# Kernel optimization log

Hardware: AMD Instinct MI355X
Metric: run time of the kernel (lower is better)

## Reference

```python
import jax, jax.numpy as jnp
import numpy as np

K = 8  # repeat(1,1,1,9) in the source forces k+1 == 9
LRELU_SLOPE = 0.01  # nn.LeakyReLU default negative slope


def knn_idx(x, k):
    """x: [B, C, N] -> indices of k nearest points [B, N, k] (largest neg sq dist)."""
    xx = jnp.sum(x * x, axis=1)                       # [B, N]
    inner = jnp.einsum('bcn,bcm->bnm', x, x)          # [B, N, N]
    neg_sq_dist = 2.0 * inner - xx[:, :, None] - xx[:, None, :]
    return jax.lax.top_k(neg_sq_dist, k)[1]           # [B, N, k]


def gather_neighbors(feat, idx):
    """feat: [B, C, N], idx: [B, N, k] -> [B, C, N, k] (grouping_operation)."""
    return jax.vmap(lambda f, i: f[:, i])(feat, idx)


def setup_inputs() -> dict:
    key = jax.random.key(0)
    k1, k2, k3 = jax.random.split(key, 3)
    B, C, N = 8, 128, 4096
    points = jax.random.normal(k1, (B, C, N), dtype=jnp.float32)
    # xavier_uniform-ish init for W [C, 1]
    limit = 1.414 * np.sqrt(6.0 / (C + 1))
    W = jax.random.uniform(k2, (C, 1), dtype=jnp.float32, minval=-limit, maxval=limit)
    conv2_w = jax.random.normal(k3, (C, C), dtype=jnp.float32) * 0.05
    return {"points": points, "W": W, "conv2_w": conv2_w}


def reference(points, W, conv2_w):
    # points: [B, C, N]
    shortcut = points
    # knn on raw (detached) features -> integer indices, no grad path
    idx = knn_idx(jax.lax.stop_gradient(points), K)            # [B, N, K]
    features = jax.nn.leaky_relu(points, LRELU_SLOPE)          # [B, C, N]
    grouped_points = gather_neighbors(features, idx)           # [B, C, N, K]
    center_points = features[:, :, :, None]                    # [B, C, N, 1]
    feats = jnp.concatenate([grouped_points, center_points], axis=3)  # [B, C, N, K+1]
    feats = jnp.transpose(feats, (0, 2, 3, 1))                 # [B, N, K+1, C]
    att = jnp.einsum('bnkc,co->bnko', feats, W)                # [B, N, K+1, 1]
    att = jax.nn.softmax(att, axis=2)                          # softmax over K+1 neighbors
    # repeat(1,1,1,9) then matmul: out[b,n,i,c] = att[b,n,i] * sum_j feats[b,n,j,c]
    # followed by mean over i -> mean_i(att) * sum_j(feats)
    s = jnp.sum(feats, axis=2)                                 # [B, N, C]
    out = jnp.mean(att, axis=2) * s                            # [B, N, C]
    out = jnp.transpose(out, (0, 2, 1)) + shortcut             # [B, C, N]
    # 1x1 conv residual branch on grouped neighbor features
    grouped_points_nn = jnp.einsum('oc,bcnk->bonk', conv2_w, grouped_points)  # [B, C, N, K]
    return (out, grouped_points_nn)
```

## Files before the change

kernel.cpp:

```cpp
#include <hip/hip_runtime.h>
#include <cstdint>
#include <cstddef>

#define BB_ 8
#define CC_ 128
#define NN_ 4096
#define KK_ 8

#define XX_OFF  0
#define IDX_OFF 32768
#define G_OFF   294912

__device__ __forceinline__ float lrelu(float v) { return v >= 0.f ? v : 0.01f * v; }

template <int S>
__device__ __forceinline__ void insert_tieup(float (&v)[S], int (&ix)[S], float d, int m) {
  if (d < v[S - 1]) return;
  bool bs[S];
#pragma unroll
  for (int s = 0; s < S; ++s) bs[s] = (v[s] > d);
#pragma unroll
  for (int s = S - 1; s >= 1; --s) {
    v[s]  = bs[s] ? v[s]  : (bs[s - 1] ? d : v[s - 1]);
    ix[s] = bs[s] ? ix[s] : (bs[s - 1] ? m : ix[s - 1]);
  }
  if (!bs[0]) { v[0] = d; ix[0] = m; }
}

template <int S>
__device__ __forceinline__ void insert_ti_desc(float (&v)[S], int (&ix)[S], float d, int m) {
  bool stay = (v[S - 1] > d) || (v[S - 1] == d && ix[S - 1] > m);
  if (stay) return;
  bool bs[S];
#pragma unroll
  for (int s = 0; s < S; ++s) bs[s] = (v[s] > d) || (v[s] == d && ix[s] > m);
#pragma unroll
  for (int s = S - 1; s >= 1; --s) {
    v[s]  = bs[s] ? v[s]  : (bs[s - 1] ? d : v[s - 1]);
    ix[s] = bs[s] ? ix[s] : (bs[s - 1] ? m : ix[s - 1]);
  }
  if (!bs[0]) { v[0] = d; ix[0] = m; }
}

__global__ void k_xx(const float* __restrict__ x, float* __restrict__ out1f) {
  int t = blockIdx.x * 256 + threadIdx.x;
  int b = t >> 12, n = t & (NN_ - 1);
  const float* p = x + ((size_t)b * CC_) * NN_ + n;
  float acc = 0.f;
  {
#pragma clang fp contract(off)
#pragma unroll
    for (int c = 0; c < CC_; ++c) {
      float v = p[(size_t)c * NN_];
      float v2 = v * v;
      acc = acc + v2;
    }
  }
  out1f[XX_OFF + t] = acc;
}

__global__ __launch_bounds__(256, 2) void k_knn(const float* __restrict__ x,
                                                float* __restrict__ out1f) {
  __shared__ __align__(16) float As[32][132];
  __shared__ __align__(16) union MB {
    float B[64][132];
    struct { float v[32 * 128]; int i[32 * 128]; } mg;
  } sb;
  __shared__ float xxm[64];

  const float* xxz = out1f + XX_OFF;
  int* idxz = (int*)(out1f + IDX_OFF);

  const int blk = blockIdx.x;
  const int b = blk >> 7;
  const int n0 = (blk & 127) << 5;
  const float* xb = x + ((size_t)b * CC_) * NN_;
  const int t = threadIdx.x;
  const int tr = t & 15, tc = t >> 4;

  {
    int r = t & 31, c0 = t >> 5;
    for (int c = c0; c < CC_; c += 8) As[r][c] = xb[(size_t)c * NN_ + n0 + r];
  }

  float xr[2];
#pragma unroll
  for (int i = 0; i < 2; ++i) xr[i] = xxz[(b << 12) + n0 + tr + 16 * i];

  float lv[2][8]; int li[2][8];
#pragma unroll
  for (int i = 0; i < 2; ++i)
#pragma unroll
    for (int s = 0; s < 8; ++s) { lv[i][s] = -INFINITY; li[i][s] = 0x7FFFFFFF; }

  for (int m0 = 0; m0 < NN_; m0 += 64) {
    __syncthreads();
    {
      int ml = t & 63, c1 = t >> 6;
      for (int c = c1; c < CC_; c += 4) sb.B[ml][c] = xb[(size_t)c * NN_ + m0 + ml];
      if (t < 64) xxm[t] = xxz[(b << 12) + m0 + t];
    }
    __syncthreads();

    float acc[2][4] = {};
#pragma unroll 8
    for (int cq = 0; cq < CC_; cq += 4) {
      float4 av[2], bv4[4];
#pragma unroll
      for (int i = 0; i < 2; ++i) av[i] = *reinterpret_cast<const float4*>(&As[tr + 16 * i][cq]);
#pragma unroll
      for (int j = 0; j < 4; ++j) bv4[j] = *reinterpret_cast<const float4*>(&sb.B[tc + 16 * j][cq]);
#pragma unroll
      for (int i = 0; i < 2; ++i)
#pragma unroll
        for (int j = 0; j < 4; ++j) {
          acc[i][j] = fmaf(av[i].x, bv4[j].x, acc[i][j]);
          acc[i][j] = fmaf(av[i].y, bv4[j].y, acc[i][j]);
          acc[i][j] = fmaf(av[i].z, bv4[j].z, acc[i][j]);
          acc[i][j] = fmaf(av[i].w, bv4[j].w, acc[i][j]);
        }
    }

#pragma unroll
    for (int j = 0; j < 4; ++j) {
      float xm = xxm[tc + 16 * j];
      int m = m0 + tc + 16 * j;
#pragma unroll
      for (int i = 0; i < 2; ++i) {
        float d = (2.0f * acc[i][j] - xr[i]) - xm;
        insert_tieup<8>(lv[i], li[i], d, m);
      }
    }
  }

  __syncthreads();
  float* candV = sb.mg.v;
  int*   candI = sb.mg.i;
#pragma unroll
  for (int i = 0; i < 2; ++i) {
    int r = tr + 16 * i;
#pragma unroll
    for (int s = 0; s < 8; ++s) {
      candV[(r << 7) + (tc << 3) + s] = lv[i][s];
      candI[(r << 7) + (tc << 3) + s] = li[i][s];
    }
  }
  __syncthreads();
  if (t < 32) {
    float bv[8]; int bi[8];
#pragma unroll
    for (int s = 0; s < 8; ++s) { bv[s] = -INFINITY; bi[s] = 0x7FFFFFFF; }
    for (int q = 0; q < 128; ++q) {
      insert_ti_desc<8>(bv, bi, candV[(t << 7) + q], candI[(t << 7) + q]);
    }
    int* op = idxz + (b << 15) + ((n0 + t) << 3);
#pragma unroll
    for (int q = 0; q < KK_; ++q) op[q] = bi[q];
  }
}

__global__ __launch_bounds__(256) void k_gemm(const float* __restrict__ x,
                                              const float* __restrict__ w2,
                                              float* __restrict__ out1f) {
  __shared__ __align__(16) float Ws[64][68];
  __shared__ __align__(16) float Fs[64][68];
  int bb = blockIdx.x >> 7;
  int r = blockIdx.x & 127;
  int o0 = (r >> 6) << 6;
  int m0 = (r & 63) << 6;
  const float* xb = x + ((size_t)bb * CC_) * NN_;
  float* gb = out1f + G_OFF + ((size_t)bb * CC_) * NN_;
  int t = threadIdx.x;
  int tm = t & 15, to = t >> 4;

  float acc[4][4] = {};
  for (int cc = 0; cc < CC_; cc += 64) {
    __syncthreads();
    {
      int cl = t & 63, q0 = t >> 6;
      for (int oo = q0; oo < 64; oo += 4) Ws[oo][cl] = w2[(o0 + oo) * CC_ + cc + cl];
      for (int c2 = q0; c2 < 64; c2 += 4) Fs[cl][c2] = lrelu(xb[(size_t)(cc + c2) * NN_ + m0 + cl]);
    }
    __syncthreads();
#pragma unroll 8
    for (int cq = 0; cq < 64; cq += 4) {
      float4 aw[4], bf[4];
#pragma unroll
      for (int i = 0; i < 4; ++i) aw[i] = *reinterpret_cast<const float4*>(&Ws[to + 16 * i][cq]);
#pragma unroll
      for (int j = 0; j < 4; ++j) bf[j] = *reinterpret_cast<const float4*>(&Fs[tm + 16 * j][cq]);
#pragma unroll
      for (int i = 0; i < 4; ++i)
#pragma unroll
        for (int j = 0; j < 4; ++j) {
          acc[i][j] = fmaf(aw[i].x, bf[j].x, acc[i][j]);
          acc[i][j] = fmaf(aw[i].y, bf[j].y, acc[i][j]);
          acc[i][j] = fmaf(aw[i].z, bf[j].z, acc[i][j]);
          acc[i][j] = fmaf(aw[i].w, bf[j].w, acc[i][j]);
        }
    }
  }
#pragma unroll
  for (int i = 0; i < 4; ++i)
#pragma unroll
    for (int j = 0; j < 4; ++j)
      gb[((size_t)(o0 + to + 16 * i)) * NN_ + m0 + tm + 16 * j] = acc[i][j];
}

__global__ void k_out0(const float* __restrict__ x, const float* __restrict__ out1f,
                       float* __restrict__ out) {
  __shared__ int idxL[512];
  int b = blockIdx.x >> 6, nt = blockIdx.x & 63;
  int n0 = nt << 6;
  int t = threadIdx.x;
  const int* ib = (const int*)(out1f + IDX_OFF) + (b << 15) + (n0 << 3);
  idxL[t] = ib[t];
  idxL[t + 256] = ib[t + 256];
  __syncthreads();
  int nl = t & 63, c0 = t >> 6;
  for (int c = c0; c < CC_; c += 4) {
    const float* row = x + ((size_t)b * CC_ + c) * NN_;
    float self = row[n0 + nl];
    float s = 0.f;
#pragma unroll
    for (int k = 0; k < KK_; ++k) s += lrelu(row[idxL[(nl << 3) + k]]);
    s += lrelu(self);
    out[((size_t)b * CC_ + c) * NN_ + n0 + nl] = fmaf(s, 1.0f / 9.0f, self);
  }
}

__global__ void k_gatherA(float* __restrict__ out1f) {
  int bc = 137 + blockIdx.x;
  int b = bc >> 7;
  const int* idxz = (const int*)(out1f + IDX_OFF) + (b << 15);
  const float* gs = out1f + G_OFF + (size_t)bc * (size_t)NN_;
  float* op = out1f + (size_t)bc * 32768;
  for (int e = threadIdx.x; e < 32768; e += 256) {
    op[e] = gs[idxz[e]];
  }
}

__global__ __launch_bounds__(256) void k_gatherB(const float* __restrict__ x,
                                                 const float* __restrict__ w2,
                                                 float* __restrict__ out1f) {
  __shared__ int idxL[512];
  __shared__ float xcols[8][128];
  int T = blockIdx.x;
  int t = threadIdx.x;
  const int* idxz = (const int*)(out1f + IDX_OFF);
  idxL[t]       = idxz[0 * 32768 + ((T * 32) << 3) + t];
  idxL[t + 256] = idxz[1 * 32768 + ((T * 32) << 3) + t];
  __syncthreads();

  for (int it = 0; it < 64; ++it) {
    int colbase = it * 8;
    {
      int cg = t >> 5, lane = t & 31;
      int col = colbase + cg;
      int bsel = col >> 8;
      int m = idxL[col];
      const float* xb = x + ((size_t)bsel * CC_) * NN_;
#pragma unroll
      for (int q = 0; q < 4; ++q) {
        int c = lane + 32 * q;
        xcols[cg][c] = lrelu(xb[(size_t)c * NN_ + m]);
      }
    }
    __syncthreads();
    {
      int cg = t >> 5, c0 = t & 31;
      int col = colbase + cg;
      int bsel = col >> 8;
      int rk = col & 255;
      int n = T * 32 + (rk >> 3);
      int k = rk & 7;
      int hmax = (bsel == 0) ? 4 : 1;
      for (int h = 0; h < hmax; ++h) {
        int c = c0 + 32 * h;
        const float* wr = w2 + c * CC_;
        float acc = 0.f;
#pragma unroll 8
        for (int cc = 0; cc < CC_; ++cc) acc = fmaf(wr[cc], xcols[cg][cc], acc);
        if (bsel == 0 || c <= 8) {
          out1f[(size_t)(bsel * CC_ + c) * 32768 + (n << 3) + k] = acc;
        }
      }
    }
    __syncthreads();
  }
}

extern "C" void kernel_launch(void* const* d_in, const int* in_sizes, int n_in,
                              void* d_out, int out_size, void* d_ws, size_t ws_size,
                              hipStream_t stream) {
  const float* x  = (const float*)d_in[0];
  const float* w2 = (const float*)d_in[2];

  float* out0  = (float*)d_out;
  float* out1f = out0 + (size_t)BB_ * CC_ * NN_;
  (void)d_ws; (void)ws_size;

  k_xx     <<<(BB_ * NN_) / 256,  256, 0, stream>>>(x, out1f);
  k_knn    <<<BB_ * (NN_ / 32),   256, 0, stream>>>(x, out1f);
  k_gemm   <<<BB_ * 128,          256, 0, stream>>>(x, w2, out1f);
  k_out0   <<<BB_ * 64,           256, 0, stream>>>(x, out1f, out0);
  k_gatherA<<<1024 - 137,         256, 0, stream>>>(out1f);
  k_gatherB<<<128,                256, 0, stream>>>(x, w2, out1f);
}
```

Measured before the change: 2.352 ms.

## Enlarge kNN query tile to 64 rows with 4x4 register blocking

The kNN distance kernel now processes 64 query points per block instead of 32. Each thread computes a 4x4 register tile, which raises arithmetic intensity and halves how often each candidate tile is reloaded from global memory per query. The candidate-merge buffer is padded to stride 129 to reduce LDS bank conflicts, and the B-tile column mapping changes to contiguous rows per thread. In exchange, shared memory grows to about 67 KB, and register pressure rises from 32 per-row top-k lists, which may cut occupancy or cause spills. The grid also shrinks to 512 blocks.

```diff
diff --git a/kernel.cpp b/kernel.cpp
--- a/kernel.cpp
+++ b/kernel.cpp
@@ -61,72 +61,76 @@
 
 __global__ __launch_bounds__(256, 2) void k_knn(const float* __restrict__ x,
                                                 float* __restrict__ out1f) {
-  __shared__ __align__(16) float As[32][132];
-  __shared__ __align__(16) union MB {
-    float B[64][132];
-    struct { float v[32 * 128]; int i[32 * 128]; } mg;
-  } sb;
-  __shared__ float xxm[64];
+  __shared__ __align__(16) union S {
+    struct {
+      float As[64][132];
+      float Bs[64][132];
+      float xxm[64];
+    } a;
+    struct { float v[64 * 129]; int i[64 * 129]; } mg;
+  } s;
 
   const float* xxz = out1f + XX_OFF;
   int* idxz = (int*)(out1f + IDX_OFF);
 
   const int blk = blockIdx.x;
-  const int b = blk >> 7;
-  const int n0 = (blk & 127) << 5;
+  const int b = blk >> 6;
+  const int n0 = (blk & 63) << 6;
   const float* xb = x + ((size_t)b * CC_) * NN_;
   const int t = threadIdx.x;
   const int tr = t & 15, tc = t >> 4;
 
   {
-    int r = t & 31, c0 = t >> 5;
-    for (int c = c0; c < CC_; c += 8) As[r][c] = xb[(size_t)c * NN_ + n0 + r];
-  }
-
-  float xr[2];
-#pragma unroll
-  for (int i = 0; i < 2; ++i) xr[i] = xxz[(b << 12) + n0 + tr + 16 * i];
-
-  float lv[2][8]; int li[2][8];
-#pragma unroll
-  for (int i = 0; i < 2; ++i)
-#pragma unroll
-    for (int s = 0; s < 8; ++s) { lv[i][s] = -INFINITY; li[i][s] = 0x7FFFFFFF; }
+    int r = t & 63, c0 = t >> 6;
+    for (int c = c0; c < CC_; c += 4) s.a.As[r][c] = xb[(size_t)c * NN_ + n0 + r];
+  }
+
+  float xr[4];
+#pragma unroll
+  for (int i = 0; i < 4; ++i) xr[i] = xxz[(b << 12) + n0 + tr + 16 * i];
+
+  float lv[4][8]; int li[4][8];
+#pragma unroll
+  for (int i = 0; i < 4; ++i)
+#pragma unroll
+    for (int q = 0; q < 8; ++q) { lv[i][q] = -INFINITY; li[i][q] = 0x7FFFFFFF; }
 
   for (int m0 = 0; m0 < NN_; m0 += 64) {
     __syncthreads();
     {
       int ml = t & 63, c1 = t >> 6;
-      for (int c = c1; c < CC_; c += 4) sb.B[ml][c] = xb[(size_t)c * NN_ + m0 + ml];
-      if (t < 64) xxm[t] = xxz[(b << 12) + m0 + t];
-    }
-    __syncthreads();
-
-    float acc[2][4] = {};
-#pragma unroll 8
+      for (int c = c1; c < CC_; c += 4) s.a.Bs[ml][c] = xb[(size_t)c * NN_ + m0 + ml];
+      if (t < 64) s.a.xxm[t] = xxz[(b << 12) + m0 + t];
+    }
+    __syncthreads();
+
+    float acc[4][4] = {};
+#pragma unroll 2
     for (int cq = 0; cq < CC_; cq += 4) {
-      float4 av[2], bv4[4];
-#pragma unroll
-      for (int i = 0; i < 2; ++i) av[i] = *reinterpret_cast<const float4*>(&As[tr + 16 * i][cq]);
-#pragma unroll
-      for (int j = 0; j < 4; ++j) bv4[j] = *reinterpret_cast<const float4*>(&sb.B[tc + 16 * j][cq]);
-#pragma unroll
-      for (int i = 0; i < 2; ++i)
+      float4 av[4], bv[4];
+#pragma unroll
+      for (int i = 0; i < 4; ++i)
+        av[i] = *reinterpret_cast<const float4*>(&s.a.As[tr + 16 * i][cq]);
+#pragma unroll
+      for (int j = 0; j < 4; ++j)
+        bv[j] = *reinterpret_cast<const float4*>(&s.a.Bs[tc * 4 + j][cq]);
+#pragma unroll
+      for (int i = 0; i < 4; ++i)
 #pragma unroll
         for (int j = 0; j < 4; ++j) {
-          acc[i][j] = fmaf(av[i].x, bv4[j].x, acc[i][j]);
-          acc[i][j] = fmaf(av[i].y, bv4[j].y, acc[i][j]);
-          acc[i][j] = fmaf(av[i].z, bv4[j].z, acc[i][j]);
-          acc[i][j] = fmaf(av[i].w, bv4[j].w, acc[i][j]);
+          acc[i][j] = fmaf(av[i].x, bv[j].x, acc[i][j]);
+          acc[i][j] = fmaf(av[i].y, bv[j].y, acc[i][j]);
+          acc[i][j] = fmaf(av[i].z, bv[j].z, acc[i][j]);
+          acc[i][j] = fmaf(av[i].w, bv[j].w, acc[i][j]);
         }
     }
 
 #pragma unroll
     for (int j = 0; j < 4; ++j) {
-      float xm = xxm[tc + 16 * j];
-      int m = m0 + tc + 16 * j;
-#pragma unroll
-      for (int i = 0; i < 2; ++i) {
+      float xm = s.a.xxm[tc * 4 + j];
+      int m = m0 + tc * 4 + j;
+#pragma unroll
+      for (int i = 0; i < 4; ++i) {
         float d = (2.0f * acc[i][j] - xr[i]) - xm;
         insert_tieup<8>(lv[i], li[i], d, m);
       }
@@ -134,24 +138,24 @@
   }
 
   __syncthreads();
-  float* candV = sb.mg.v;
-  int*   candI = sb.mg.i;
-#pragma unroll
-  for (int i = 0; i < 2; ++i) {
-    int r = tr + 16 * i;
-#pragma unroll
-    for (int s = 0; s < 8; ++s) {
-      candV[(r << 7) + (tc << 3) + s] = lv[i][s];
-      candI[(r << 7) + (tc << 3) + s] = li[i][s];
+#pragma unroll
+  for (int i = 0; i < 4; ++i) {
+    int base = (tr + 16 * i) * 129 + (tc << 3);
+#pragma unroll
+    for (int q = 0; q < 8; ++q) {
+      s.mg.v[base + q] = lv[i][q];
+      s.mg.i[base + q] = li[i][q];
     }
   }
   __syncthreads();
-  if (t < 32) {
+  if (t < 64) {
     float bv[8]; int bi[8];
 #pragma unroll
-    for (int s = 0; s < 8; ++s) { bv[s] = -INFINITY; bi[s] = 0x7FFFFFFF; }
+    for (int q = 0; q < 8; ++q) { bv[q] = -INFINITY; bi[q] = 0x7FFFFFFF; }
+    const float* cv = s.mg.v + t * 129;
+    const int*   ci = s.mg.i + t * 129;
     for (int q = 0; q < 128; ++q) {
-      insert_ti_desc<8>(bv, bi, candV[(t << 7) + q], candI[(t << 7) + q]);
+      insert_ti_desc<8>(bv, bi, cv[q], ci[q]);
     }
     int* op = idxz + (b << 15) + ((n0 + t) << 3);
 #pragma unroll
@@ -301,7 +305,7 @@
   (void)d_ws; (void)ws_size;
 
   k_xx     <<<(BB_ * NN_) / 256,  256, 0, stream>>>(x, out1f);
-  k_knn    <<<BB_ * (NN_ / 32),   256, 0, stream>>>(x, out1f);
+  k_knn    <<<BB_ * (NN_ / 64),   256, 0, stream>>>(x, out1f);
   k_gemm   <<<BB_ * 128,          256, 0, stream>>>(x, w2, out1f);
   k_out0   <<<BB_ * 64,           256, 0, stream>>>(x, out1f, out0);
   k_gatherA<<<1024 - 137,         256, 0, stream>>>(out1f);
```

Result: faster. 2.182 ms (-7.2%).

## Split kNN into bf16 MFMA candidate filter plus exact fp32 rerank

Applied to the files above, without the earlier changes.

Replaces the fp32 SIMT distance GEMM and top-k kernel with a two-stage scheme. A prep kernel writes transposed fp32 and bf16 copies of the points. A bf16 MFMA filter kernel then keeps 8 candidates per 16-column lane group, giving 256 candidates per row. An exact kernel recomputes fp32 distances for those candidates and merges the per-lane top-8 lists with shuffles. This moves the O(N^2 C) work onto matrix cores, at the cost of extra scratch traffic and a risk that bf16 rounding drops a true neighbor from the candidate set.

```diff
diff --git a/kernel.cpp b/kernel.cpp
--- a/kernel.cpp
+++ b/kernel.cpp
@@ -7,11 +7,23 @@
 #define NN_ 4096
 #define KK_ 8
 
-#define XX_OFF  0
-#define IDX_OFF 32768
-#define G_OFF   294912
+#define XX_OFF   0
+#define IDX_OFF  32768
+#define G_OFF    294912
+#define XT_OFF   16777216
+#define XH_OFF   20971520
+#define CAND_OFF 23068672
+
+typedef __attribute__((ext_vector_type(8))) short bf16x8;
+typedef __attribute__((ext_vector_type(4))) float f32x4;
 
 __device__ __forceinline__ float lrelu(float v) { return v >= 0.f ? v : 0.01f * v; }
+
+__device__ __forceinline__ unsigned short f2bf(float f) {
+  unsigned int u = __float_as_uint(f);
+  unsigned int r = (u + 0x7FFFu + ((u >> 16) & 1u)) >> 16;
+  return (unsigned short)r;
+}
 
 template <int S>
 __device__ __forceinline__ void insert_tieup(float (&v)[S], int (&ix)[S], float d, int m) {
@@ -40,6 +52,30 @@
     ix[s] = bs[s] ? ix[s] : (bs[s - 1] ? m : ix[s - 1]);
   }
   if (!bs[0]) { v[0] = d; ix[0] = m; }
+}
+
+__global__ __launch_bounds__(256) void k_prep(const float* __restrict__ x,
+                                              float* __restrict__ out1f) {
+  __shared__ float Ls[64][132];
+  int b = blockIdx.x >> 6, mt = blockIdx.x & 63;
+  int m0 = mt << 6;
+  int t = threadIdx.x;
+  const float* xb = x + ((size_t)b * CC_) * NN_;
+  {
+    int ml = t & 63, c0 = t >> 6;
+    for (int c = c0; c < CC_; c += 4) Ls[ml][c] = xb[(size_t)c * NN_ + m0 + ml];
+  }
+  __syncthreads();
+  float* xTb = out1f + XT_OFF + (size_t)(b << 12) * CC_;
+  unsigned short* xhb = (unsigned short*)(out1f + XH_OFF) + (size_t)(b << 12) * CC_;
+  {
+    int cl = t & 127, r0 = t >> 7;
+    for (int r = r0; r < 64; r += 2) {
+      float v = Ls[r][cl];
+      xTb[(size_t)(m0 + r) * CC_ + cl] = v;
+      xhb[(size_t)(m0 + r) * CC_ + cl] = f2bf(v);
+    }
+  }
 }
 
 __global__ void k_xx(const float* __restrict__ x, float* __restrict__ out1f) {
@@ -59,103 +95,118 @@
   out1f[XX_OFF + t] = acc;
 }
 
-__global__ __launch_bounds__(256, 2) void k_knn(const float* __restrict__ x,
-                                                float* __restrict__ out1f) {
-  __shared__ __align__(16) float As[32][132];
-  __shared__ __align__(16) union MB {
-    float B[64][132];
-    struct { float v[32 * 128]; int i[32 * 128]; } mg;
-  } sb;
-  __shared__ float xxm[64];
-
+__global__ __launch_bounds__(256) void k_filter(float* __restrict__ out1f) {
   const float* xxz = out1f + XX_OFF;
+  const unsigned short* xhz = (const unsigned short*)(out1f + XH_OFF);
+  int* candz = (int*)(out1f + CAND_OFF);
+
+  const int blk = blockIdx.x;
+  const int b  = blk >> 7;
+  const int nt = (blk >> 1) & 63;
+  const int h  = blk & 1;
+  const int t = threadIdx.x;
+  const int w = t >> 6, l = t & 63;
+  const int lj = l & 15, lq = l >> 4;
+  const int n0w = (nt << 6) + (w << 4);
+
+  const unsigned short* xhb = xhz + (size_t)(b << 12) * CC_;
+  const float* xxb = xxz + (b << 12);
+
+  bf16x8 afr[4];
+#pragma unroll
+  for (int kk = 0; kk < 4; ++kk)
+    afr[kk] = *(const bf16x8*)(xhb + (size_t)(n0w + lj) * CC_ + 32 * kk + 8 * lq);
+
+  float lv[4][8]; int li[4][8];
+#pragma unroll
+  for (int r = 0; r < 4; ++r)
+#pragma unroll
+    for (int s = 0; s < 8; ++s) { lv[r][s] = -INFINITY; li[r][s] = 0x7FFFFFFF; }
+
+  for (int mt2 = 0; mt2 < 128; ++mt2) {
+    const int m0 = (h << 11) + (mt2 << 4);
+    const unsigned short* bp = xhb + (size_t)(m0 + lj) * CC_ + 8 * lq;
+    bf16x8 bfr[4];
+#pragma unroll
+    for (int kk = 0; kk < 4; ++kk) bfr[kk] = *(const bf16x8*)(bp + 32 * kk);
+    float xm = xxb[m0 + lj];
+
+    f32x4 c = {0.f, 0.f, 0.f, 0.f};
+#pragma unroll
+    for (int kk = 0; kk < 4; ++kk)
+      c = __builtin_amdgcn_mfma_f32_16x16x32_bf16(afr[kk], bfr[kk], c, 0, 0, 0);
+
+    const int m = m0 + lj;
+#pragma unroll
+    for (int r = 0; r < 4; ++r) {
+      float s = fmaf(2.0f, c[r], -xm);
+      insert_tieup<8>(lv[r], li[r], s, m);
+    }
+  }
+
+#pragma unroll
+  for (int r = 0; r < 4; ++r) {
+    size_t rowg = (size_t)(b << 12) + n0w + 4 * lq + r;
+    int* cp = candz + rowg * 256 + h * 128 + lj * 8;
+#pragma unroll
+    for (int s = 0; s < 8; ++s) cp[s] = li[r][s];
+  }
+}
+
+__global__ __launch_bounds__(256) void k_exact(float* __restrict__ out1f) {
+  const float* xxz = out1f + XX_OFF;
+  const float* xTz = out1f + XT_OFF;
+  const int* candz = (const int*)(out1f + CAND_OFF);
   int* idxz = (int*)(out1f + IDX_OFF);
 
-  const int blk = blockIdx.x;
-  const int b = blk >> 7;
-  const int n0 = (blk & 127) << 5;
-  const float* xb = x + ((size_t)b * CC_) * NN_;
   const int t = threadIdx.x;
-  const int tr = t & 15, tc = t >> 4;
-
-  {
-    int r = t & 31, c0 = t >> 5;
-    for (int c = c0; c < CC_; c += 8) As[r][c] = xb[(size_t)c * NN_ + n0 + r];
-  }
-
-  float xr[2];
-#pragma unroll
-  for (int i = 0; i < 2; ++i) xr[i] = xxz[(b << 12) + n0 + tr + 16 * i];
-
-  float lv[2][8]; int li[2][8];
-#pragma unroll
-  for (int i = 0; i < 2; ++i)
-#pragma unroll
-    for (int s = 0; s < 8; ++s) { lv[i][s] = -INFINITY; li[i][s] = 0x7FFFFFFF; }
-
-  for (int m0 = 0; m0 < NN_; m0 += 64) {
-    __syncthreads();
-    {
-      int ml = t & 63, c1 = t >> 6;
-      for (int c = c1; c < CC_; c += 4) sb.B[ml][c] = xb[(size_t)c * NN_ + m0 + ml];
-      if (t < 64) xxm[t] = xxz[(b << 12) + m0 + t];
-    }
-    __syncthreads();
-
-    float acc[2][4] = {};
+  const int w = t >> 6, l = t & 63;
+  const int lr = l >> 4, lj = l & 15;
+  const size_t rowg = (size_t)blockIdx.x * 16 + w * 4 + lr;
+  const int b = (int)(rowg >> 12);
+  const int nloc = (int)(rowg & (NN_ - 1));
+  const float* xTb = xTz + (size_t)(b << 12) * CC_;
+  const float xr = xxz[rowg];
+
+  const float4* ap = (const float4*)(xTb + (size_t)nloc * CC_);
+  const int* cp = candz + rowg * 256 + lj * 16;
+
+  float ev[8]; int ei[8];
+#pragma unroll
+  for (int s = 0; s < 8; ++s) { ev[s] = -INFINITY; ei[s] = 0x7FFFFFFF; }
+
+  for (int j = 0; j < 16; ++j) {
+    const int m = cp[j];
+    const float4* bp4 = (const float4*)(xTb + (size_t)m * CC_);
+    float acc = 0.f;
 #pragma unroll 8
-    for (int cq = 0; cq < CC_; cq += 4) {
-      float4 av[2], bv4[4];
-#pragma unroll
-      for (int i = 0; i < 2; ++i) av[i] = *reinterpret_cast<const float4*>(&As[tr + 16 * i][cq]);
-#pragma unroll
-      for (int j = 0; j < 4; ++j) bv4[j] = *reinterpret_cast<const float4*>(&sb.B[tc + 16 * j][cq]);
-#pragma unroll
-      for (int i = 0; i < 2; ++i)
-#pragma unroll
-        for (int j = 0; j < 4; ++j) {
-          acc[i][j] = fmaf(av[i].x, bv4[j].x, acc[i][j]);
-          acc[i][j] = fmaf(av[i].y, bv4[j].y, acc[i][j]);
-          acc[i][j] = fmaf(av[i].z, bv4[j].z, acc[i][j]);
-          acc[i][j] = fmaf(av[i].w, bv4[j].w, acc[i][j]);
-        }
-    }
-
-#pragma unroll
-    for (int j = 0; j < 4; ++j) {
-      float xm = xxm[tc + 16 * j];
-      int m = m0 + tc + 16 * j;
-#pragma unroll
-      for (int i = 0; i < 2; ++i) {
-        float d = (2.0f * acc[i][j] - xr[i]) - xm;
-        insert_tieup<8>(lv[i], li[i], d, m);
-      }
-    }
-  }
-
-  __syncthreads();
-  float* candV = sb.mg.v;
-  int*   candI = sb.mg.i;
-#pragma unroll
-  for (int i = 0; i < 2; ++i) {
-    int r = tr + 16 * i;
+    for (int g = 0; g < 32; ++g) {
+      float4 a4 = ap[g], b4 = bp4[g];
+      acc = fmaf(a4.x, b4.x, acc);
+      acc = fmaf(a4.y, b4.y, acc);
+      acc = fmaf(a4.z, b4.z, acc);
+      acc = fmaf(a4.w, b4.w, acc);
+    }
+    float d = (2.0f * acc - xr) - xxz[(size_t)(b << 12) + m];
+    insert_ti_desc<8>(ev, ei, d, m);
+  }
+
+#pragma unroll
+  for (int mk = 1; mk <= 8; mk <<= 1) {
+    float pv[8]; int pi[8];
 #pragma unroll
     for (int s = 0; s < 8; ++s) {
-      candV[(r << 7) + (tc << 3) + s] = lv[i][s];
-      candI[(r << 7) + (tc << 3) + s] = li[i][s];
-    }
-  }
-  __syncthreads();
-  if (t < 32) {
-    float bv[8]; int bi[8];
-#pragma unroll
-    for (int s = 0; s < 8; ++s) { bv[s] = -INFINITY; bi[s] = 0x7FFFFFFF; }
-    for (int q = 0; q < 128; ++q) {
-      insert_ti_desc<8>(bv, bi, candV[(t << 7) + q], candI[(t << 7) + q]);
-    }
-    int* op = idxz + (b << 15) + ((n0 + t) << 3);
-#pragma unroll
-    for (int q = 0; q < KK_; ++q) op[q] = bi[q];
+      pv[s] = __shfl_xor(ev[s], mk, 64);
+      pi[s] = __shfl_xor(ei[s], mk, 64);
+    }
+#pragma unroll
+    for (int s = 0; s < 8; ++s) insert_ti_desc<8>(ev, ei, pv[s], pi[s]);
+  }
+
+  if (lj == 0) {
+    int* op = idxz + rowg * 8;
+#pragma unroll
+    for (int q = 0; q < KK_; ++q) op[q] = ei[q];
   }
 }
 
@@ -275,8 +326,8 @@
       int n = T * 32 + (rk >> 3);
       int k = rk & 7;
       int hmax = (bsel == 0) ? 4 : 1;
-      for (int h = 0; h < hmax; ++h) {
-        int c = c0 + 32 * h;
+      for (int hh = 0; hh < hmax; ++hh) {
+        int c = c0 + 32 * hh;
         const float* wr = w2 + c * CC_;
         float acc = 0.f;
 #pragma unroll 8
@@ -300,8 +351,10 @@
   float* out1f = out0 + (size_t)BB_ * CC_ * NN_;
   (void)d_ws; (void)ws_size;
 
+  k_prep   <<<BB_ * 64,           256, 0, stream>>>(x, out1f);
   k_xx     <<<(BB_ * NN_) / 256,  256, 0, stream>>>(x, out1f);
-  k_knn    <<<BB_ * (NN_ / 32),   256, 0, stream>>>(x, out1f);
+  k_filter <<<BB_ * 128,          256, 0, stream>>>(out1f);
+  k_exact  <<<2048,               256, 0, stream>>>(out1f);
   k_gemm   <<<BB_ * 128,          256, 0, stream>>>(x, w2, out1f);
   k_out0   <<<BB_ * 64,           256, 0, stream>>>(x, out1f, out0);
   k_gatherA<<<1024 - 137,         256, 0, stream>>>(out1f);
```

Measured after the change: 2.303 ms. -2.1%, faster.
